# Performance work log

Measured on AMD Instinct MI355X. Metric: run time of the kernel, lower is better.

Reference implementation:

```python
import jax, jax.numpy as jnp
import numpy as np

COORD_DIM, PARAM_DIM, H, L, O = 3, 8, 128, 5, 5
B, N_PTS = 16, 50000


def setup_inputs() -> dict:
    key = jax.random.key(0)
    ks = jax.random.split(key, 16)
    def w(k, shape, fan_in):
        return jax.random.normal(k, shape, dtype=jnp.float32) / np.sqrt(fan_in)
    inp = {
        "coords": jax.random.normal(ks[0], (B, N_PTS, COORD_DIM), dtype=jnp.float32),
        "params": jax.random.normal(ks[1], (B, PARAM_DIM), dtype=jnp.float32),
        # branch MLP: param_dim -> H (x5 hidden, rowdy tanh) -> H*O
        "branch_W0": w(ks[2], (PARAM_DIM, H), PARAM_DIM),
        "branch_b0": jnp.zeros((H,), jnp.float32),
        "branch_Wh": w(ks[3], (L - 1, H, H), H),
        "branch_bh": jnp.zeros((L - 1, H), jnp.float32),
        "branch_alpha": jnp.ones((L, H), jnp.float32),
        "branch_Wf": w(ks[4], (H, H * O), H),
        "branch_bf": jnp.zeros((H * O,), jnp.float32),
        # trunk: coord_dim -> H (x5, FiLM by branch cumsum, rowdy tanh) -> H
        "trunk_W0": w(ks[5], (COORD_DIM, H), COORD_DIM),
        "trunk_b0": jnp.zeros((H,), jnp.float32),
        "trunk_Wh": w(ks[6], (L - 1, H, H), H),
        "trunk_bh": jnp.zeros((L - 1, H), jnp.float32),
        "trunk_alpha": jnp.ones((L, H), jnp.float32),
        "trunk_Wf": w(ks[7], (H, H), H),
        "trunk_bf": jnp.zeros((H,), jnp.float32),
    }
    return inp


def reference(coords, params, branch_W0, branch_b0, branch_Wh, branch_bh,
              branch_alpha, branch_Wf, branch_bf, trunk_W0, trunk_b0,
              trunk_Wh, trunk_bh, trunk_alpha, trunk_Wf, trunk_bf):
    # ---- branch MLP with RowdyActivation, keeping hidden outputs ----
    h = branch_alpha[0] * jnp.tanh(params @ branch_W0 + branch_b0)  # (B,H)
    hiddens = [h]
    for i in range(L - 1):
        h = branch_alpha[i + 1] * jnp.tanh(h @ branch_Wh[i] + branch_bh[i])
        hiddens.append(h)
    branch_out = h @ branch_Wf + branch_bf  # (B, H*O)
    # cumulative sums S_i = sum_{j<=i} hidden_j
    S = [hiddens[0]]
    for i in range(1, L):
        S.append(hiddens[i] + S[-1])
    # ---- trunk with FiLM modulation ----
    x = coords @ trunk_W0 + trunk_b0                       # (B,n,H)
    x = trunk_alpha[0] * jnp.tanh(x * S[0][:, None, :])
    for i in range(1, L):
        x = x @ trunk_Wh[i - 1] + trunk_bh[i - 1]
        x = trunk_alpha[i] * jnp.tanh(x * S[i][:, None, :])
    YL = x @ trunk_Wf + trunk_bf                           # (B,n,H)
    ZL = branch_out.reshape(B, O, H)                       # (B,O,H)
    # out[b,n,o] = sum_h ZL[b,o,h] * YL[b,n,h]  (tiled matmul, no (B,n,O,H) temp)
    return jnp.einsum('bnh,boh->bno', YL, ZL)
```

## Files before the change

kernel.cpp:

```cpp
#include <hip/hip_runtime.h>
#include <math.h>

#define H      128
#define LNUM   5
#define ONUM   5
#define BATCH  16
#define NPTS   50000
#define TP     64
#define XROW   152

#define K2LOG2E 2.8853900817779268f

typedef _Float16      half8    __attribute__((ext_vector_type(8)));
typedef float         floatx4  __attribute__((ext_vector_type(4)));
typedef unsigned int  uint2v   __attribute__((ext_vector_type(2)));
typedef unsigned int  uint4v   __attribute__((ext_vector_type(4)));
typedef unsigned short ushort8_t __attribute__((ext_vector_type(8)));

static __device__ __forceinline__ unsigned short f2h(float f) {
    _Float16 h = (_Float16)f;
    return __builtin_bit_cast(unsigned short, h);
}
static __device__ __forceinline__ unsigned int packh(float a, float b) {
    return (unsigned int)f2h(a) | ((unsigned int)f2h(b) << 16);
}

__global__ __launch_bounds__(512)
void fold_kernel(const float* __restrict__ params,
                 const float* __restrict__ bW0, const float* __restrict__ bb0,
                 const float* __restrict__ bWh, const float* __restrict__ bbh,
                 const float* __restrict__ balpha,
                 const float* __restrict__ bWf, const float* __restrict__ bbf,
                 const float* __restrict__ tW0, const float* __restrict__ tb0,
                 const float* __restrict__ tWh, const float* __restrict__ tbh,
                 const float* __restrict__ tWf, const float* __restrict__ talpha,
                 const float* __restrict__ tbf,
                 unsigned short* __restrict__ w0s, unsigned short* __restrict__ whs,
                 unsigned short* __restrict__ wcomb, float* __restrict__ bcomb,
                 float* __restrict__ binit) {
    const int b = blockIdx.x, l = blockIdx.y, t = threadIdx.x;
    __shared__ float hbuf[H];
    __shared__ float Sneed[H];
    __shared__ float pbuf[8];
    __shared__ float zl_sh[ONUM][H];
    if (t < 8) pbuf[t] = params[b * 8 + t];
    __syncthreads();

    float scum = 0.0f;
    if (t < H) {
        float acc = bb0[t];
        for (int k = 0; k < 8; ++k) acc += pbuf[k] * bW0[k * H + t];
        float h = balpha[t] * tanhf(acc);
        hbuf[t] = h;
        scum = h;
        if (l == 0) Sneed[t] = scum;
    }
    for (int i = 1; i < LNUM; ++i) {
        __syncthreads();
        float hn = 0.0f;
        if (t < H) {
            const float* Wl = bWh + (i - 1) * H * H;
            float a2 = bbh[(i - 1) * H + t];
            for (int k = 0; k < H; ++k) a2 += hbuf[k] * Wl[k * H + t];
            hn = balpha[i * H + t] * tanhf(a2);
        }
        __syncthreads();
        if (t < H) {
            hbuf[t] = hn;
            scum += hn;
            if (i == l) Sneed[t] = scum;
        }
    }
    __syncthreads();

    if (l == 5) {
        for (int idx = t; idx < ONUM * H; idx += 512) {
            int o = idx >> 7, hh = idx & 127;
            float z = bbf[o * H + hh];
            for (int k = 0; k < H; ++k) z += hbuf[k] * bWf[k * (H * ONUM) + o * H + hh];
            zl_sh[o][hh] = z;
        }
        __syncthreads();
        for (int j = t; j < 16 * H; j += 512) {
            int o = j >> 7, f = j & 127;
            float v = 0.0f;
            if (o < ONUM) {
                const float* wfr = tWf + f * H;
                float s = 0.0f;
                for (int h = 0; h < H; ++h) s += wfr[h] * zl_sh[o][h];
                v = talpha[4 * H + f] * s;
            }
            wcomb[b * 16 * H + j] = f2h(v);
        }
        if (t < 16) {
            float v = 0.0f;
            if (t < ONUM)
                for (int h = 0; h < H; ++h) v += tbf[h] * zl_sh[t][h];
            bcomb[b * 16 + t] = v;
        }
    } else if (l == 0) {
        if (t < H) binit[(b * LNUM + 0) * H + t] = K2LOG2E * Sneed[t] * tb0[t];
        unsigned int* dst = (unsigned int*)(w0s + b * H * 32);
        for (int j = t; j < H * 16; j += 512) {
            int f = j >> 4, k0 = (j & 15) << 1;
            float s = K2LOG2E * Sneed[f];
            float v0 = (k0 < 3)     ? s * tW0[k0 * H + f]       : 0.0f;
            float v1 = (k0 + 1 < 3) ? s * tW0[(k0 + 1) * H + f] : 0.0f;
            dst[j] = packh(v0, v1);
        }
    } else {
        if (t < H) binit[(b * LNUM + l) * H + t] = K2LOG2E * Sneed[t] * tbh[(l - 1) * H + t];
        const float* Wsrc = tWh + (l - 1) * H * H;
        unsigned int* dst = (unsigned int*)(whs + (b * 4 + (l - 1)) * H * H);
        for (int j = t; j < H * H / 2; j += 512) {
            int f = j >> 6, k0 = (j & 63) << 1;
            float s = K2LOG2E * Sneed[f];
            dst[j] = packh(s * Wsrc[k0 * H + f] * talpha[(l - 1) * H + k0],
                           s * Wsrc[(k0 + 1) * H + f] * talpha[(l - 1) * H + k0 + 1]);
        }
    }
}

__global__ __launch_bounds__(256, 4)
void trunk_kernel(const float* __restrict__ coords,
                  const unsigned short* __restrict__ w0s,
                  const unsigned short* __restrict__ whs,
                  const float* __restrict__ binit,
                  const unsigned short* __restrict__ wcomb,
                  const float* __restrict__ bcomb,
                  float* __restrict__ out) {
    const int b    = blockIdx.y;
    const int n0   = blockIdx.x * TP;
    const int tid  = threadIdx.x;
    const int lane = tid & 63;
    const int w    = tid >> 6;
    const int q    = lane >> 4;
    const int c    = lane & 15;
    const int mq   = w * 32;

    __shared__ unsigned short xs[TP * XROW];

    int valid = NPTS - n0; if (valid > TP) valid = TP;
    {
        int p = tid >> 2, part = tid & 3;
        uint4v z = {0, 0, 0, 0};
        if (part == 0) {
            float c0 = 0.f, c1 = 0.f, c2 = 0.f;
            if (p < valid) {
                const float* cp = coords + ((size_t)b * NPTS + n0 + p) * 3;
                c0 = cp[0]; c1 = cp[1]; c2 = cp[2];
            }
            z.x = __builtin_bit_cast(unsigned int, __builtin_amdgcn_cvt_pkrtz(c0, c1));
            z.y = __builtin_bit_cast(unsigned int, __builtin_amdgcn_cvt_pkrtz(c2, 0.0f));
        }
        *(uint4v*)&xs[p * XROW + part * 8] = z;
    }
    __syncthreads();

    floatx4 acc[2][4];

    #pragma unroll
    for (int mt = 0; mt < 2; ++mt) {
        floatx4 bi4 = *(const floatx4*)&binit[(b * LNUM + 0) * H + mq + mt * 16 + q * 4];
        #pragma unroll
        for (int nt = 0; nt < 4; ++nt) acc[mt][nt] = bi4;
    }
    {
        const unsigned short* w0b = w0s + b * H * 32;
        half8 af[2], bfr[4];
        #pragma unroll
        for (int mt = 0; mt < 2; ++mt)
            af[mt] = __builtin_bit_cast(half8,
                *(const ushort8_t*)&w0b[(mq + mt * 16 + c) * 32 + q * 8]);
        #pragma unroll
        for (int nt = 0; nt < 4; ++nt)
            bfr[nt] = __builtin_bit_cast(half8,
                *(const ushort8_t*)&xs[(nt * 16 + c) * XROW + q * 8]);
        #pragma unroll
        for (int mt = 0; mt < 2; ++mt)
            #pragma unroll
            for (int nt = 0; nt < 4; ++nt)
                acc[mt][nt] = __builtin_amdgcn_mfma_f32_16x16x32_f16(af[mt], bfr[nt], acc[mt][nt], 0, 0, 0);
    }
    __syncthreads();
    #pragma unroll
    for (int mt = 0; mt < 2; ++mt) {
        int f0 = mq + mt * 16 + q * 4;
        #pragma unroll
        for (int nt = 0; nt < 4; ++nt) {
            int pt = nt * 16 + c;
            floatx4 v = acc[mt][nt];
            #pragma unroll
            for (int r = 0; r < 4; ++r) {
                float e  = __builtin_amdgcn_exp2f(v[r]);
                float rc = __builtin_amdgcn_rcpf(e + 1.0f);
                v[r] = __builtin_fmaf(-2.0f, rc, 1.0f);
            }
            uint2v u;
            u.x = __builtin_bit_cast(unsigned int, __builtin_amdgcn_cvt_pkrtz(v[0], v[1]));
            u.y = __builtin_bit_cast(unsigned int, __builtin_amdgcn_cvt_pkrtz(v[2], v[3]));
            *(uint2v*)&xs[pt * XROW + f0] = u;
        }
    }

    for (int l = 1; l <= 4; ++l) {
        const unsigned short* wl = whs + (b * 4 + (l - 1)) * H * H;
        #pragma unroll
        for (int mt = 0; mt < 2; ++mt) {
            floatx4 bi4 = *(const floatx4*)&binit[(b * LNUM + l) * H + mq + mt * 16 + q * 4];
            #pragma unroll
            for (int nt = 0; nt < 4; ++nt) acc[mt][nt] = bi4;
        }
        __syncthreads();
        #pragma unroll
        for (int s = 0; s < 4; ++s) {
            half8 af[2], bfr[4];
            #pragma unroll
            for (int mt = 0; mt < 2; ++mt)
                af[mt] = __builtin_bit_cast(half8,
                    *(const ushort8_t*)&wl[(mq + mt * 16 + c) * H + s * 32 + q * 8]);
            #pragma unroll
            for (int nt = 0; nt < 4; ++nt)
                bfr[nt] = __builtin_bit_cast(half8,
                    *(const ushort8_t*)&xs[(nt * 16 + c) * XROW + s * 32 + q * 8]);
            #pragma unroll
            for (int mt = 0; mt < 2; ++mt)
                #pragma unroll
                for (int nt = 0; nt < 4; ++nt)
                    acc[mt][nt] = __builtin_amdgcn_mfma_f32_16x16x32_f16(af[mt], bfr[nt], acc[mt][nt], 0, 0, 0);
        }
        __syncthreads();
        #pragma unroll
        for (int mt = 0; mt < 2; ++mt) {
            int f0 = mq + mt * 16 + q * 4;
            #pragma unroll
            for (int nt = 0; nt < 4; ++nt) {
                int pt = nt * 16 + c;
                floatx4 v = acc[mt][nt];
                #pragma unroll
                for (int r = 0; r < 4; ++r) {
                    float e  = __builtin_amdgcn_exp2f(v[r]);
                    float rc = __builtin_amdgcn_rcpf(e + 1.0f);
                    v[r] = __builtin_fmaf(-2.0f, rc, 1.0f);
                }
                uint2v u;
                u.x = __builtin_bit_cast(unsigned int, __builtin_amdgcn_cvt_pkrtz(v[0], v[1]));
                u.y = __builtin_bit_cast(unsigned int, __builtin_amdgcn_cvt_pkrtz(v[2], v[3]));
                *(uint2v*)&xs[pt * XROW + f0] = u;
            }
        }
    }
    __syncthreads();

    {
        floatx4 oacc = *(const floatx4*)&bcomb[b * 16 + q * 4];
        const unsigned short* wc = wcomb + b * 16 * H;
        #pragma unroll
        for (int s = 0; s < 4; ++s) {
            half8 af = __builtin_bit_cast(half8,
                *(const ushort8_t*)&wc[c * H + s * 32 + q * 8]);
            half8 bfr = __builtin_bit_cast(half8,
                *(const ushort8_t*)&xs[(w * 16 + c) * XROW + s * 32 + q * 8]);
            oacc = __builtin_amdgcn_mfma_f32_16x16x32_f16(af, bfr, oacc, 0, 0, 0);
        }
        int pt = n0 + w * 16 + c;
        if (pt < NPTS) {
            float* op = out + ((size_t)b * NPTS + pt) * ONUM;
            if (q == 0) {
                op[0] = oacc[0]; op[1] = oacc[1];
                op[2] = oacc[2]; op[3] = oacc[3];
            } else if (q == 1) {
                op[4] = oacc[0];
            }
        }
    }
}

extern "C" void kernel_launch(void* const* d_in, const int* in_sizes, int n_in,
                              void* d_out, int out_size, void* d_ws, size_t ws_size,
                              hipStream_t stream) {
    const float* coords       = (const float*)d_in[0];
    const float* params       = (const float*)d_in[1];
    const float* branch_W0    = (const float*)d_in[2];
    const float* branch_b0    = (const float*)d_in[3];
    const float* branch_Wh    = (const float*)d_in[4];
    const float* branch_bh    = (const float*)d_in[5];
    const float* branch_alpha = (const float*)d_in[6];
    const float* branch_Wf    = (const float*)d_in[7];
    const float* branch_bf    = (const float*)d_in[8];
    const float* trunk_W0     = (const float*)d_in[9];
    const float* trunk_b0     = (const float*)d_in[10];
    const float* trunk_Wh     = (const float*)d_in[11];
    const float* trunk_bh     = (const float*)d_in[12];
    const float* trunk_alpha  = (const float*)d_in[13];
    const float* trunk_Wf     = (const float*)d_in[14];
    const float* trunk_bf     = (const float*)d_in[15];
    float* out = (float*)d_out;

    char* ws = (char*)d_ws;
    float*          binit = (float*)(ws + 0);
    unsigned short* wcomb = (unsigned short*)(ws + 40960);
    float*          bcomb = (float*)(ws + 106496);
    unsigned short* w0s   = (unsigned short*)(ws + 107520);
    unsigned short* whs   = (unsigned short*)(ws + 238592);

    fold_kernel<<<dim3(BATCH, 6), 512, 0, stream>>>(params, branch_W0, branch_b0,
                                                    branch_Wh, branch_bh, branch_alpha,
                                                    branch_Wf, branch_bf,
                                                    trunk_W0, trunk_b0, trunk_Wh, trunk_bh,
                                                    trunk_Wf, trunk_alpha, trunk_bf,
                                                    w0s, whs, wcomb, bcomb, binit);
    trunk_kernel<<<dim3((NPTS + TP - 1) / TP, BATCH), 256, 0, stream>>>(
        coords, w0s, whs, binit, wcomb, bcomb, out);
}
```

Before: 353.9 us.

## Double trunk point tile to 128 points per block, reusing weight fragments

```diff
diff --git a/kernel.cpp b/kernel.cpp
--- a/kernel.cpp
+++ b/kernel.cpp
@@ -6,7 +6,7 @@
 #define ONUM   5
 #define BATCH  16
 #define NPTS   50000
-#define TP     64
+#define TP     128
 #define XROW   152
 
 #define K2LOG2E 2.8853900817779268f
@@ -121,7 +121,7 @@
     }
 }
 
-__global__ __launch_bounds__(256, 4)
+__global__ __launch_bounds__(256, 3)
 void trunk_kernel(const float* __restrict__ coords,
                   const unsigned short* __restrict__ w0s,
                   const unsigned short* __restrict__ whs,
@@ -142,52 +142,58 @@
 
     int valid = NPTS - n0; if (valid > TP) valid = TP;
     {
-        int p = tid >> 2, part = tid & 3;
-        uint4v z = {0, 0, 0, 0};
-        if (part == 0) {
+        int p = tid >> 1, hh = tid & 1;
+        if (hh == 0) {
             float c0 = 0.f, c1 = 0.f, c2 = 0.f;
             if (p < valid) {
                 const float* cp = coords + ((size_t)b * NPTS + n0 + p) * 3;
                 c0 = cp[0]; c1 = cp[1]; c2 = cp[2];
             }
+            uint4v z;
             z.x = __builtin_bit_cast(unsigned int, __builtin_amdgcn_cvt_pkrtz(c0, c1));
             z.y = __builtin_bit_cast(unsigned int, __builtin_amdgcn_cvt_pkrtz(c2, 0.0f));
-        }
-        *(uint4v*)&xs[p * XROW + part * 8] = z;
-    }
-    __syncthreads();
-
-    floatx4 acc[2][4];
+            z.z = 0; z.w = 0;
+            *(uint4v*)&xs[p * XROW + 0] = z;
+            uint4v zz = {0, 0, 0, 0};
+            *(uint4v*)&xs[p * XROW + 8] = zz;
+        } else {
+            uint4v zz = {0, 0, 0, 0};
+            *(uint4v*)&xs[p * XROW + 16] = zz;
+            *(uint4v*)&xs[p * XROW + 24] = zz;
+        }
+    }
+    __syncthreads();
+
+    floatx4 acc[2][8];
 
     #pragma unroll
     for (int mt = 0; mt < 2; ++mt) {
         floatx4 bi4 = *(const floatx4*)&binit[(b * LNUM + 0) * H + mq + mt * 16 + q * 4];
         #pragma unroll
-        for (int nt = 0; nt < 4; ++nt) acc[mt][nt] = bi4;
+        for (int nt = 0; nt < 8; ++nt) acc[mt][nt] = bi4;
     }
     {
         const unsigned short* w0b = w0s + b * H * 32;
-        half8 af[2], bfr[4];
+        half8 af[2];
         #pragma unroll
         for (int mt = 0; mt < 2; ++mt)
             af[mt] = __builtin_bit_cast(half8,
                 *(const ushort8_t*)&w0b[(mq + mt * 16 + c) * 32 + q * 8]);
         #pragma unroll
-        for (int nt = 0; nt < 4; ++nt)
-            bfr[nt] = __builtin_bit_cast(half8,
+        for (int nt = 0; nt < 8; ++nt) {
+            half8 bfr = __builtin_bit_cast(half8,
                 *(const ushort8_t*)&xs[(nt * 16 + c) * XROW + q * 8]);
-        #pragma unroll
-        for (int mt = 0; mt < 2; ++mt)
-            #pragma unroll
-            for (int nt = 0; nt < 4; ++nt)
-                acc[mt][nt] = __builtin_amdgcn_mfma_f32_16x16x32_f16(af[mt], bfr[nt], acc[mt][nt], 0, 0, 0);
+            #pragma unroll
+            for (int mt = 0; mt < 2; ++mt)
+                acc[mt][nt] = __builtin_amdgcn_mfma_f32_16x16x32_f16(af[mt], bfr, acc[mt][nt], 0, 0, 0);
+        }
     }
     __syncthreads();
     #pragma unroll
     for (int mt = 0; mt < 2; ++mt) {
         int f0 = mq + mt * 16 + q * 4;
         #pragma unroll
-        for (int nt = 0; nt < 4; ++nt) {
+        for (int nt = 0; nt < 8; ++nt) {
             int pt = nt * 16 + c;
             floatx4 v = acc[mt][nt];
             #pragma unroll
@@ -209,32 +215,31 @@
         for (int mt = 0; mt < 2; ++mt) {
             floatx4 bi4 = *(const floatx4*)&binit[(b * LNUM + l) * H + mq + mt * 16 + q * 4];
             #pragma unroll
-            for (int nt = 0; nt < 4; ++nt) acc[mt][nt] = bi4;
+            for (int nt = 0; nt < 8; ++nt) acc[mt][nt] = bi4;
         }
         __syncthreads();
         #pragma unroll
         for (int s = 0; s < 4; ++s) {
-            half8 af[2], bfr[4];
+            half8 af[2];
             #pragma unroll
             for (int mt = 0; mt < 2; ++mt)
                 af[mt] = __builtin_bit_cast(half8,
                     *(const ushort8_t*)&wl[(mq + mt * 16 + c) * H + s * 32 + q * 8]);
             #pragma unroll
-            for (int nt = 0; nt < 4; ++nt)
-                bfr[nt] = __builtin_bit_cast(half8,
+            for (int nt = 0; nt < 8; ++nt) {
+                half8 bfr = __builtin_bit_cast(half8,
                     *(const ushort8_t*)&xs[(nt * 16 + c) * XROW + s * 32 + q * 8]);
-            #pragma unroll
-            for (int mt = 0; mt < 2; ++mt)
                 #pragma unroll
-                for (int nt = 0; nt < 4; ++nt)
-                    acc[mt][nt] = __builtin_amdgcn_mfma_f32_16x16x32_f16(af[mt], bfr[nt], acc[mt][nt], 0, 0, 0);
+                for (int mt = 0; mt < 2; ++mt)
+                    acc[mt][nt] = __builtin_amdgcn_mfma_f32_16x16x32_f16(af[mt], bfr, acc[mt][nt], 0, 0, 0);
+            }
         }
         __syncthreads();
         #pragma unroll
         for (int mt = 0; mt < 2; ++mt) {
             int f0 = mq + mt * 16 + q * 4;
             #pragma unroll
-            for (int nt = 0; nt < 4; ++nt) {
+            for (int nt = 0; nt < 8; ++nt) {
                 int pt = nt * 16 + c;
                 floatx4 v = acc[mt][nt];
                 #pragma unroll
@@ -253,24 +258,31 @@
     __syncthreads();
 
     {
-        floatx4 oacc = *(const floatx4*)&bcomb[b * 16 + q * 4];
+        floatx4 bc = *(const floatx4*)&bcomb[b * 16 + q * 4];
+        floatx4 oacc[2] = {bc, bc};
         const unsigned short* wc = wcomb + b * 16 * H;
         #pragma unroll
         for (int s = 0; s < 4; ++s) {
             half8 af = __builtin_bit_cast(half8,
                 *(const ushort8_t*)&wc[c * H + s * 32 + q * 8]);
-            half8 bfr = __builtin_bit_cast(half8,
-                *(const ushort8_t*)&xs[(w * 16 + c) * XROW + s * 32 + q * 8]);
-            oacc = __builtin_amdgcn_mfma_f32_16x16x32_f16(af, bfr, oacc, 0, 0, 0);
-        }
-        int pt = n0 + w * 16 + c;
-        if (pt < NPTS) {
-            float* op = out + ((size_t)b * NPTS + pt) * ONUM;
-            if (q == 0) {
-                op[0] = oacc[0]; op[1] = oacc[1];
-                op[2] = oacc[2]; op[3] = oacc[3];
-            } else if (q == 1) {
-                op[4] = oacc[0];
+            #pragma unroll
+            for (int nt = 0; nt < 2; ++nt) {
+                half8 bfr = __builtin_bit_cast(half8,
+                    *(const ushort8_t*)&xs[(w * 32 + nt * 16 + c) * XROW + s * 32 + q * 8]);
+                oacc[nt] = __builtin_amdgcn_mfma_f32_16x16x32_f16(af, bfr, oacc[nt], 0, 0, 0);
+            }
+        }
+        #pragma unroll
+        for (int nt = 0; nt < 2; ++nt) {
+            int pt = n0 + w * 32 + nt * 16 + c;
+            if (pt < NPTS) {
+                float* op = out + ((size_t)b * NPTS + pt) * ONUM;
+                if (q == 0) {
+                    op[0] = oacc[nt][0]; op[1] = oacc[nt][1];
+                    op[2] = oacc[nt][2]; op[3] = oacc[nt][3];
+                } else if (q == 1) {
+                    op[4] = oacc[nt][0];
+                }
             }
         }
     }
```

Result: faster. 283.9 us (-19.8%).
